# Performance work log

Measured on AMD Instinct MI355X. Metric: run time of the kernel, lower is better.

The kernel has to match this reference:

```python
import jax, jax.numpy as jnp
import numpy as np

B, T, N, D = 16, 24, 2048, 64
L, K = 2, 3  # num_layers, cheb_k


def setup_inputs() -> dict:
    key = jax.random.key(0)
    ks = jax.random.split(key, 6)
    x = jax.random.normal(ks[0], (B, T, N, D), dtype=jnp.float32)
    init_state = jnp.zeros((L, B, N, D), dtype=jnp.float32)
    adj = jax.random.uniform(ks[1], (N, N), dtype=jnp.float32)
    adj = adj / jnp.sum(adj, axis=-1, keepdims=True)  # row-normalized adjacency
    cin = 2 * D
    Wg = jax.random.normal(ks[2], (L, K, cin, 2 * D), dtype=jnp.float32) * (1.0 / np.sqrt(K * cin))
    bg = jnp.zeros((L, 2 * D), dtype=jnp.float32)
    Wu = jax.random.normal(ks[3], (L, K, cin, D), dtype=jnp.float32) * (1.0 / np.sqrt(K * cin))
    bu = jnp.zeros((L, D), dtype=jnp.float32)
    return {"x": x, "init_state": init_state, "adj_matrix": adj,
            "Wg": Wg, "bg": bg, "Wu": Wu, "bu": bu}


def _cheb_supports(adj, k):
    # T0=I, T1=A, Tk = 2*A@T_{k-1} - T_{k-2}
    n = adj.shape[0]
    sup = [jnp.eye(n, dtype=adj.dtype), adj]
    for _ in range(2, k):
        sup.append(2.0 * adj @ sup[-1] - sup[-2])
    return jnp.stack(sup[:k], axis=0)  # [K, N, N]


def _gconv(xs, supports, W, b):
    # xs: [B,N,Cin], supports: [K,N,N], W: [K,Cin,Cout]
    xg = jnp.einsum('knm,bmc->bknc', supports, xs)
    return jnp.einsum('bknc,kco->bno', xg, W) + b


def _cell(x_t, state, supports, Wg_l, bg_l, Wu_l, bu_l):
    ins = jnp.concatenate([x_t, state], axis=-1)  # [B,N,2D]
    zr = jax.nn.sigmoid(_gconv(ins, supports, Wg_l, bg_l))
    z, r = jnp.split(zr, 2, axis=-1)
    cand_in = jnp.concatenate([x_t, z * state], axis=-1)
    hc = jnp.tanh(_gconv(cand_in, supports, Wu_l, bu_l))
    return r * state + (1.0 - r) * hc


def reference(x, init_state, adj_matrix, Wg, bg, Wu, bu):
    supports = _cheb_supports(adj_matrix, K)
    current = x  # [B,T,N,D]
    hiddens = []
    for l in range(L):
        def step(state, x_t, l=l):
            new = _cell(x_t, state, supports, Wg[l], bg[l], Wu[l], bu[l])
            return new, new
        last, seq = jax.lax.scan(step, init_state[l], jnp.swapaxes(current, 0, 1))
        hiddens.append(last)
        current = x + jnp.swapaxes(seq, 0, 1)  # residual over the stacked states
    return current, jnp.stack(hiddens, axis=0)
```

## Files before the change

### kernel.cpp

```cpp
#include <hip/hip_runtime.h>
#include <hip/hip_bf16.h>
#include <math.h>

typedef __bf16 bf16x8 __attribute__((ext_vector_type(8)));
typedef float f32x4 __attribute__((ext_vector_type(4)));
typedef __hip_bfloat16 bf16s;

constexpr int kB = 16, kT = 24, kN = 2048, kD = 64;
constexpr size_t kBND = (size_t)kB * kN * kD;

struct Slot { const void* p0; const void* p1; int astr0, trow0, astr1, trow1, type; };
struct Slots6 { Slot s[6]; };
struct DiffGrp { const bf16s* src; bf16s* oA; bf16s* oA2; };
struct Diff2P { const bf16s* S0; const bf16s* S1; DiffGrp g[2]; int ytPerGrp; };

__device__ __forceinline__ void async_copy16(void* lds, const void* g) {
  __builtin_amdgcn_global_load_lds((const __attribute__((address_space(1))) void*)g,
                                   (__attribute__((address_space(3))) void*)lds,
                                   16, 0, 0);
}


__device__ __forceinline__ void diff2_tile(
    const bf16s* __restrict__ S0, const bf16s* __restrict__ S1,
    const bf16s* __restrict__ src, bf16s* oA, bf16s* oA2,
    int m0, int c0, bf16s* lds)
{
  bf16s* lA  = lds;
  bf16s* lA2 = lds + 4096;
  bf16s* lB  = lds + 8192;
  const int tid = threadIdx.x, lane = tid & 63, wave = tid >> 6;
  const int wm = (wave >> 1) * 32, wn = (wave & 1) * 64;
  const int ra = tid >> 3;
  const int cs = ((tid & 7) ^ (ra & 7)) * 8;
  const int rk0 = ((lane >> 4) ^ (lane & 7)) * 8;
  const int rk1 = ((4 + (lane >> 4)) ^ (lane & 7)) * 8;

  f32x4 acc[2][2][4];
  const f32x4 zero = {0.f, 0.f, 0.f, 0.f};
#pragma unroll
  for (int s = 0; s < 2; ++s)
#pragma unroll
    for (int i = 0; i < 2; ++i)
#pragma unroll
      for (int j = 0; j < 4; ++j) acc[s][i][j] = zero;

  for (int k0 = 0; k0 < 2048; k0 += 64) {
#pragma unroll
    for (int i = 0; i < 2; ++i) {
      async_copy16(lA  + (size_t)(i * 256 + tid) * 8,
                   S0 + (size_t)(m0 + i * 32 + ra) * 2048 + k0 + cs);
      async_copy16(lA2 + (size_t)(i * 256 + tid) * 8,
                   S1 + (size_t)(m0 + i * 32 + ra) * 2048 + k0 + cs);
    }
#pragma unroll
    for (int i = 0; i < 4; ++i)
      async_copy16(lB + (size_t)(i * 256 + tid) * 8,
                   src + (size_t)(c0 + i * 32 + ra) * 2048 + k0 + cs);
    __syncthreads();
#pragma unroll
    for (int ks = 0; ks < 2; ++ks) {
      const int rk = ks ? rk1 : rk0;
      bf16x8 av0[2], av1[2], bv[4];
#pragma unroll
      for (int f = 0; f < 2; ++f) {
        av0[f] = *(const bf16x8*)(lA  + (size_t)(wm + f * 16 + (lane & 15)) * 64 + rk);
        av1[f] = *(const bf16x8*)(lA2 + (size_t)(wm + f * 16 + (lane & 15)) * 64 + rk);
      }
#pragma unroll
      for (int f = 0; f < 4; ++f)
        bv[f] = *(const bf16x8*)(lB + (size_t)(wn + f * 16 + (lane & 15)) * 64 + rk);
#pragma unroll
      for (int i = 0; i < 2; ++i)
#pragma unroll
        for (int j = 0; j < 4; ++j) {
          acc[0][i][j] = __builtin_amdgcn_mfma_f32_16x16x32_bf16(av0[i], bv[j], acc[0][i][j], 0, 0, 0);
          acc[1][i][j] = __builtin_amdgcn_mfma_f32_16x16x32_bf16(av1[i], bv[j], acc[1][i][j], 0, 0, 0);
        }
    }
    __syncthreads();
  }

  const int rq = (lane >> 4) * 4, cl = lane & 15;
#pragma unroll
  for (int sp = 0; sp < 2; ++sp) {
    bf16s* out = sp ? oA2 : oA;
#pragma unroll
    for (int fm = 0; fm < 2; ++fm)
#pragma unroll
      for (int fn = 0; fn < 4; ++fn)
#pragma unroll
        for (int q = 0; q < 4; ++q) {
          int gm = m0 + wm + fm * 16 + rq + q;
          int gc = c0 + wn + fn * 16 + cl;
          out[((size_t)(gc >> 6) * 2048 + gm) * 64 + (gc & 63)] =
              __float2bfloat16(acc[sp][fm][fn][q]);
        }
  }
}

__global__ __launch_bounds__(256) void k_diff2(Diff2P p)
{
  __shared__ bf16s lds[16384];
  const int mb = blockIdx.x;
  const int grp = blockIdx.y / p.ytPerGrp;
  const int cb = blockIdx.y - grp * p.ytPerGrp;
  const DiffGrp G = p.g[grp];
  diff2_tile(p.S0, p.S1, G.src, G.oA, G.oA2, mb * 64, cb * 128, lds);
}

__device__ __forceinline__ void diff_core(
    const bf16s* __restrict__ S, const bf16s* __restrict__ Bsrc,
    int m0, int c0, bf16s* lA, bf16s* lB, f32x4 (&acc)[4][4])
{
  const int tid = threadIdx.x, lane = tid & 63, wave = tid >> 6;
  const int wm = (wave >> 1) * 64, wn = (wave & 1) * 64;
  const f32x4 zero = {0.f, 0.f, 0.f, 0.f};
#pragma unroll
  for (int i = 0; i < 4; ++i)
#pragma unroll
    for (int j = 0; j < 4; ++j) acc[i][j] = zero;

  const int ra = tid >> 3;
  const int cs = ((tid & 7) ^ (ra & 7)) * 8;
  const int rk0 = ((lane >> 4) ^ (lane & 7)) * 8;
  const int rk1 = ((4 + (lane >> 4)) ^ (lane & 7)) * 8;

  for (int k0 = 0; k0 < 2048; k0 += 64) {
#pragma unroll
    for (int i = 0; i < 4; ++i) {
      async_copy16(lA + (size_t)(i * 256 + tid) * 8,
                   S + (size_t)(m0 + i * 32 + ra) * 2048 + k0 + cs);
      async_copy16(lB + (size_t)(i * 256 + tid) * 8,
                   Bsrc + (size_t)(c0 + i * 32 + ra) * 2048 + k0 + cs);
    }
    __syncthreads();
#pragma unroll
    for (int ks = 0; ks < 2; ++ks) {
      const int rk = ks ? rk1 : rk0;
      bf16x8 av[4], bv[4];
#pragma unroll
      for (int f = 0; f < 4; ++f) {
        av[f] = *(const bf16x8*)(lA + (size_t)(wm + f * 16 + (lane & 15)) * 64 + rk);
        bv[f] = *(const bf16x8*)(lB + (size_t)(wn + f * 16 + (lane & 15)) * 64 + rk);
      }
#pragma unroll
      for (int i = 0; i < 4; ++i)
#pragma unroll
        for (int j = 0; j < 4; ++j)
          acc[i][j] = __builtin_amdgcn_mfma_f32_16x16x32_bf16(av[i], bv[j], acc[i][j], 0, 0, 0);
    }
    __syncthreads();
  }
}

__global__ __launch_bounds__(256) void k_a2(
    const bf16s* __restrict__ A, const bf16s* __restrict__ AT, bf16s* A2)
{
  __shared__ bf16s lA[128 * 64];
  __shared__ bf16s lB[128 * 64];
  const int m0 = blockIdx.x * 128, n0 = blockIdx.y * 128;
  f32x4 acc[4][4];
  diff_core(A, AT, m0, n0, lA, lB, acc);
  const int lane = threadIdx.x & 63, wave = threadIdx.x >> 6;
  const int wm = (wave >> 1) * 64, wn = (wave & 1) * 64;
  const int rq = (lane >> 4) * 4, cl = lane & 15;
#pragma unroll
  for (int fm = 0; fm < 4; ++fm)
#pragma unroll
    for (int fn = 0; fn < 4; ++fn)
#pragma unroll
      for (int q = 0; q < 4; ++q) {
        int gm = m0 + wm + fm * 16 + rq + q;
        int gc = n0 + wn + fn * 16 + cl;
        A2[(size_t)gm * 2048 + gc] = __float2bfloat16(2.f * acc[fm][fn][q] - (gm == gc ? 1.f : 0.f));
      }
}

template<int BN>
__device__ __forceinline__ void small_core(
    const Slots6& sl, int m0, const bf16s* __restrict__ W,
    bf16s* lA, bf16s* lB, f32x4 (&acc)[4][BN / 32])
{
  const int tid = threadIdx.x, lane = tid & 63, wave = tid >> 6;
  const int wm = (wave >> 1) * 64, wn = (wave & 1) * (BN / 2);
  const f32x4 zero = {0.f, 0.f, 0.f, 0.f};
#pragma unroll
  for (int i = 0; i < 4; ++i)
#pragma unroll
    for (int j = 0; j < BN / 32; ++j) acc[i][j] = zero;

  const int ra = tid >> 3;
  const int cs = ((tid & 7) ^ (ra & 7)) * 8;
  const int rk0 = ((lane >> 4) ^ (lane & 7)) * 8;
  const int rk1 = ((4 + (lane >> 4)) ^ (lane & 7)) * 8;

#pragma unroll
  for (int ks = 0; ks < 6; ++ks) {
    const Slot sd = sl.s[ks];
    if (sd.type == 0) {
      const bf16s* base = (const bf16s*)sd.p0;
#pragma unroll
      for (int i = 0; i < 4; ++i) {
        int row = m0 + i * 32 + ra;
        size_t roff = ((size_t)(row >> 11) * sd.astr0 + sd.trow0 + (row & 2047)) * 64 + cs;
        async_copy16(lA + (size_t)(i * 256 + tid) * 8, base + roff);
      }
    } else if (sd.type == 1) {
#pragma unroll
      for (int i = 0; i < 4; ++i) {
        int row = m0 + i * 32 + ra;
        size_t roff = ((size_t)(row >> 11) * sd.astr0 + sd.trow0 + (row & 2047)) * 64 + cs;
        const float4* q0 = (const float4*)((const float*)sd.p0 + roff);
        float4 a = q0[0], b = q0[1];
        union { bf16x8 v; bf16s h[8]; } u;
        u.h[0] = __float2bfloat16(a.x); u.h[1] = __float2bfloat16(a.y);
        u.h[2] = __float2bfloat16(a.z); u.h[3] = __float2bfloat16(a.w);
        u.h[4] = __float2bfloat16(b.x); u.h[5] = __float2bfloat16(b.y);
        u.h[6] = __float2bfloat16(b.z); u.h[7] = __float2bfloat16(b.w);
        *(bf16x8*)(lA + (size_t)(i * 256 + tid) * 8) = u.v;
      }
    } else {
#pragma unroll
      for (int i = 0; i < 4; ++i) {
        int row = m0 + i * 32 + ra;
        size_t r0o = ((size_t)(row >> 11) * sd.astr0 + sd.trow0 + (row & 2047)) * 64 + cs;
        size_t r1o = ((size_t)(row >> 11) * sd.astr1 + sd.trow1 + (row & 2047)) * 64 + cs;
        union { bf16x8 v; bf16s h[8]; } a, b, o;
        a.v = *(const bf16x8*)((const bf16s*)sd.p0 + r0o);
        b.v = *(const bf16x8*)((const bf16s*)sd.p1 + r1o);
#pragma unroll
        for (int j = 0; j < 8; ++j)
          o.h[j] = __float2bfloat16(__bfloat162float(a.h[j]) + __bfloat162float(b.h[j]));
        *(bf16x8*)(lA + (size_t)(i * 256 + tid) * 8) = o.v;
      }
    }
#pragma unroll
    for (int i = 0; i < BN / 32; ++i)
      async_copy16(lB + (size_t)(i * 256 + tid) * 8,
                   W + (size_t)(i * 32 + ra) * 384 + ks * 64 + cs);
    __syncthreads();
#pragma unroll
    for (int kss = 0; kss < 2; ++kss) {
      const int rk = kss ? rk1 : rk0;
      bf16x8 av[4], bv[BN / 32];
#pragma unroll
      for (int f = 0; f < 4; ++f)
        av[f] = *(const bf16x8*)(lA + (size_t)(wm + f * 16 + (lane & 15)) * 64 + rk);
#pragma unroll
      for (int f = 0; f < BN / 32; ++f)
        bv[f] = *(const bf16x8*)(lB + (size_t)(wn + f * 16 + (lane & 15)) * 64 + rk);
#pragma unroll
      for (int i = 0; i < 4; ++i)
#pragma unroll
        for (int j = 0; j < BN / 32; ++j)
          acc[i][j] = __builtin_amdgcn_mfma_f32_16x16x32_bf16(av[i], bv[j], acc[i][j], 0, 0, 0);
    }
    __syncthreads();
  }
}

struct LayerG {
  Slots6 sl; const bf16s* W; const float* bias;
  const float* h; bf16s* zh; bf16s* zhT; float* r;
};
__global__ __launch_bounds__(256) void k_gate(LayerG A, LayerG B, int nA)
{
  __shared__ bf16s lA[128 * 64];
  __shared__ bf16s lB[128 * 64];
  const int bx = blockIdx.x;
  const bool isA = bx < nA;
  const LayerG L = isA ? A : B;
  const int m0 = (isA ? bx : bx - nA) * 128;
  f32x4 acc[4][4];
  small_core<128>(L.sl, m0, L.W, lA, lB, acc);
  const int lane = threadIdx.x & 63, wave = threadIdx.x >> 6;
  const int wm = (wave >> 1) * 64, wn = (wave & 1) * 64;
  const int rq = (lane >> 4) * 4, cl = lane & 15;
#pragma unroll
  for (int fm = 0; fm < 4; ++fm)
#pragma unroll
    for (int fn = 0; fn < 4; ++fn) {
      const int o = wn + fn * 16 + cl;
      const float bias = L.bias[o];
#pragma unroll
      for (int q = 0; q < 4; ++q) {
        size_t gm = (size_t)m0 + wm + fm * 16 + rq + q;
        float s = 1.f / (1.f + expf(-(acc[fm][fn][q] + bias)));
        if (o < 64) {
          float zh = s * L.h[gm * 64 + o];
          L.zh[gm * 64 + o] = __float2bfloat16(zh);
          L.zhT[((size_t)((gm >> 11) * 64 + o)) * 2048 + (gm & 2047)] = __float2bfloat16(zh);
        } else {
          L.r[gm * 64 + (o - 64)] = s;
        }
      }
    }
}

__device__ __forceinline__ Slot Sb_d(const void* p0, int astr, int trow) {
  return Slot{p0, nullptr, astr, trow, 0, 0, 0};
}
__device__ __forceinline__ Slot Sf_d(const void* p0, int astr, int trow) {
  return Slot{p0, nullptr, astr, trow, 0, 0, 1};
}
__device__ __forceinline__ Slot S2_d(const void* p0, const void* p1, int astr1, int trow1) {
  return Slot{p0, p1, 2048, 0, astr1, trow1, 2};
}

struct CandP {
  const bf16s *A, *A2;
  const bf16s *zhT0, *zhT1;
  bf16s *sZ0, *sA2Z0, *sZ1, *sA2Z1;
  const float *x;
  const bf16s *zhbf0, *zhbf1, *x1prev;
  const bf16s *AxF, *A2xF, *sAh0, *sA2h0;
  const bf16s *WuT; const float *bu;
  const float *r32_0, *r32_1;
  float *h32_0, *h32_1;
  bf16s *hT0, *hT1, *hbf0, *hbf1;
  bf16s *x1cur;
  float *outCur, *outHid;
  int tA, tB, aA, aB;
};

__global__ __launch_bounds__(256, 2) void k_dcand(CandP P)
{
  __shared__ bf16s lds[16384];
  const int layer = blockIdx.x >> 8;
  if (layer ? !P.aB : !P.aA) return;
  const int lin = blockIdx.x & 255;
  const int mb = (lin & 7) | (((lin >> 6) & 3) << 3);
  const int cb = (lin >> 3) & 7;
  const int m0 = mb * 64, c0 = cb * 128, b0 = cb * 2;
  const int t = layer ? P.tB : P.tA;

  const int tid = threadIdx.x, lane = tid & 63, wave = tid >> 6;
  const int ra = tid >> 3;
  const int cs = ((tid & 7) ^ (ra & 7)) * 8;
  const int rk0 = ((lane >> 4) ^ (lane & 7)) * 8;
  const int rk1 = ((4 + (lane >> 4)) ^ (lane & 7)) * 8;

  diff2_tile(P.A, P.A2, layer ? P.zhT1 : P.zhT0,
             layer ? P.sZ1 : P.sZ0, layer ? P.sA2Z1 : P.sA2Z0,
             m0, c0, lds);
  __syncthreads();

  Slots6 sl;
  if (!layer) {
    sl.s[0] = Sf_d(P.x, kT * 2048, P.tA * 2048);
    sl.s[1] = Sb_d(P.zhbf0, 2048, 0);
    sl.s[2] = Sb_d(P.AxF, kT * 2048, P.tA * 2048);
    sl.s[3] = Sb_d(P.sZ0, 2048, 0);
    sl.s[4] = Sb_d(P.A2xF, kT * 2048, P.tA * 2048);
    sl.s[5] = Sb_d(P.sA2Z0, 2048, 0);
  } else {
    sl.s[0] = Sb_d(P.x1prev, 2048, 0);
    sl.s[1] = Sb_d(P.zhbf1, 2048, 0);
    sl.s[2] = S2_d(P.sAh0, P.AxF, kT * 2048, P.tB * 2048);
    sl.s[3] = Sb_d(P.sZ1, 2048, 0);
    sl.s[4] = S2_d(P.sA2h0, P.A2xF, kT * 2048, P.tB * 2048);
    sl.s[5] = Sb_d(P.sA2Z1, 2048, 0);
  }
  const bf16s* W = P.WuT + (size_t)layer * 64 * 384;
  const float* bias = P.bu + layer * 64;

  bf16s* gA = lds;
  bf16s* gB = lds + 8192;
  const int wmG = (wave >> 1) * 64, wnG = (wave & 1) * 32;
  f32x4 gacc[4][2];
  const f32x4 zero = {0.f, 0.f, 0.f, 0.f};
#pragma unroll
  for (int i = 0; i < 4; ++i)
#pragma unroll
    for (int j = 0; j < 2; ++j) gacc[i][j] = zero;

#pragma unroll
  for (int ks = 0; ks < 6; ++ks) {
    const Slot sd = sl.s[ks];
    if (sd.type == 0) {
      const bf16s* base = (const bf16s*)sd.p0;
#pragma unroll
      for (int i = 0; i < 4; ++i) {
        int vrow = i * 32 + ra;
        size_t gm = (size_t)(b0 + (vrow >> 6)) * 2048 + m0 + (vrow & 63);
        size_t roff = ((gm >> 11) * sd.astr0 + sd.trow0 + (gm & 2047)) * 64 + cs;
        async_copy16(gA + (size_t)(i * 256 + tid) * 8, base + roff);
      }
    } else if (sd.type == 1) {
#pragma unroll
      for (int i = 0; i < 4; ++i) {
        int vrow = i * 32 + ra;
        size_t gm = (size_t)(b0 + (vrow >> 6)) * 2048 + m0 + (vrow & 63);
        size_t roff = ((gm >> 11) * sd.astr0 + sd.trow0 + (gm & 2047)) * 64 + cs;
        const float4* q0 = (const float4*)((const float*)sd.p0 + roff);
        float4 a = q0[0], b = q0[1];
        union { bf16x8 v; bf16s h[8]; } u;
        u.h[0] = __float2bfloat16(a.x); u.h[1] = __float2bfloat16(a.y);
        u.h[2] = __float2bfloat16(a.z); u.h[3] = __float2bfloat16(a.w);
        u.h[4] = __float2bfloat16(b.x); u.h[5] = __float2bfloat16(b.y);
        u.h[6] = __float2bfloat16(b.z); u.h[7] = __float2bfloat16(b.w);
        *(bf16x8*)(gA + (size_t)(i * 256 + tid) * 8) = u.v;
      }
    } else {
#pragma unroll
      for (int i = 0; i < 4; ++i) {
        int vrow = i * 32 + ra;
        size_t gm = (size_t)(b0 + (vrow >> 6)) * 2048 + m0 + (vrow & 63);
        size_t r0o = ((gm >> 11) * sd.astr0 + sd.trow0 + (gm & 2047)) * 64 + cs;
        size_t r1o = ((gm >> 11) * sd.astr1 + sd.trow1 + (gm & 2047)) * 64 + cs;
        union { bf16x8 v; bf16s h[8]; } a, b, o;
        a.v = *(const bf16x8*)((const bf16s*)sd.p0 + r0o);
        b.v = *(const bf16x8*)((const bf16s*)sd.p1 + r1o);
#pragma unroll
        for (int j = 0; j < 8; ++j)
          o.h[j] = __float2bfloat16(__bfloat162float(a.h[j]) + __bfloat162float(b.h[j]));
        *(bf16x8*)(gA + (size_t)(i * 256 + tid) * 8) = o.v;
      }
    }
#pragma unroll
    for (int i = 0; i < 2; ++i)
      async_copy16(gB + (size_t)(i * 256 + tid) * 8,
                   W + (size_t)(i * 32 + ra) * 384 + ks * 64 + cs);
    __syncthreads();
#pragma unroll
    for (int kss = 0; kss < 2; ++kss) {
      const int rk = kss ? rk1 : rk0;
      bf16x8 av[4], bv[2];
#pragma unroll
      for (int f = 0; f < 4; ++f)
        av[f] = *(const bf16x8*)(gA + (size_t)(wmG + f * 16 + (lane & 15)) * 64 + rk);
#pragma unroll
      for (int f = 0; f < 2; ++f)
        bv[f] = *(const bf16x8*)(gB + (size_t)(wnG + f * 16 + (lane & 15)) * 64 + rk);
#pragma unroll
      for (int i = 0; i < 4; ++i)
#pragma unroll
        for (int j = 0; j < 2; ++j)
          gacc[i][j] = __builtin_amdgcn_mfma_f32_16x16x32_bf16(av[i], bv[j], gacc[i][j], 0, 0, 0);
    }
    __syncthreads();
  }

  const float* r32 = layer ? P.r32_1 : P.r32_0;
  float* h32 = layer ? P.h32_1 : P.h32_0;
  bf16s* hT  = layer ? P.hT1  : P.hT0;
  bf16s* hbf = layer ? P.hbf1 : P.hbf0;
  const int rq = (lane >> 4) * 4, cl = lane & 15;
#pragma unroll
  for (int fm = 0; fm < 4; ++fm)
#pragma unroll
    for (int fn = 0; fn < 2; ++fn) {
      const int d = wnG + fn * 16 + cl;
      const float bias_d = bias[d];
#pragma unroll
      for (int q = 0; q < 4; ++q) {
        int vrow = wmG + fm * 16 + rq + q;
        size_t gm = (size_t)(b0 + (vrow >> 6)) * 2048 + m0 + (vrow & 63);
        float hc = tanhf(gacc[fm][fn][q] + bias_d);
        float r = r32[gm * 64 + d];
        float h = h32[gm * 64 + d];
        float hn = r * h + (1.f - r) * hc;
        h32[gm * 64 + d] = hn;
        int b = (int)(gm >> 11), n = (int)(gm & 2047);
        hT[((size_t)(b * 64 + d)) * 2048 + n] = __float2bfloat16(hn);
        hbf[gm * 64 + d] = __float2bfloat16(hn);
        size_t xi = (((size_t)b * kT + t) * 2048 + n) * 64 + d;
        if (!layer) {
          P.x1cur[gm * 64 + d] = __float2bfloat16(P.x[xi] + hn);
          if (t == kT - 1) P.outHid[gm * 64 + d] = hn;
        } else {
          P.outCur[xi] = P.x[xi] + hn;
          if (t == kT - 1) (P.outHid + kBND)[gm * 64 + d] = hn;
        }
      }
    }
}

__global__ __launch_bounds__(256) void transpose_cvt(
    const float* in, bf16s* out, int nrows, int ncols,
    size_t in_ostride, size_t out_ostride)
{
  __shared__ float tile[64][65];
  const int r0 = blockIdx.x * 64, c0 = blockIdx.y * 64;
  in  += (size_t)blockIdx.z * in_ostride;
  out += (size_t)blockIdx.z * out_ostride;
  const int tx = threadIdx.x & 63, ty = threadIdx.x >> 6;
#pragma unroll
  for (int i = 0; i < 64; i += 4)
    tile[ty + i][tx] = in[(size_t)(r0 + ty + i) * ncols + c0 + tx];
  __syncthreads();
#pragma unroll
  for (int i = 0; i < 64; i += 4)
    out[(size_t)(c0 + ty + i) * nrows + r0 + tx] = __float2bfloat16(tile[tx][ty + i]);
}

__global__ __launch_bounds__(256) void k_cvt(const float* in, bf16s* out, int n)
{
  int i = blockIdx.x * 256 + threadIdx.x;
  if (i < n) out[i] = __float2bfloat16(in[i]);
}

__global__ __launch_bounds__(256) void k_repack(
    const float* Wg, const float* Wu, bf16s* WgT, bf16s* WuT)
{
  int idx = blockIdx.x * 256 + threadIdx.x;
  if (idx < 2 * 3 * 128 * 128) {
    int o = idx & 127, cin = (idx >> 7) & 127, k = (idx >> 14) % 3, l = idx / 49152;
    WgT[((size_t)(l * 128 + o)) * 384 + (2 * k + (cin >> 6)) * 64 + (cin & 63)] =
        __float2bfloat16(Wg[idx]);
  }
  if (idx < 2 * 3 * 128 * 64) {
    int o = idx & 63, cin = (idx >> 6) & 127, k = (idx >> 13) % 3, l = idx / 24576;
    WuT[((size_t)(l * 64 + o)) * 384 + (2 * k + (cin >> 6)) * 64 + (cin & 63)] =
        __float2bfloat16(Wu[idx]);
  }
}

__global__ __launch_bounds__(256) void init_layer(
    const float* ist_l, float* h32, bf16s* hT, bf16s* h_bf)
{
  size_t idx = (size_t)blockIdx.x * 256 + threadIdx.x;
  if (idx >= kBND) return;
  int d = (int)(idx & 63);
  size_t row = idx >> 6;
  int n = (int)(row & 2047), b = (int)(row >> 11);
  float h = ist_l[idx];
  h32[idx] = h;
  hT[((size_t)(b * 64 + d)) * 2048 + n] = __float2bfloat16(h);
  h_bf[idx] = __float2bfloat16(h);
}

extern "C" void kernel_launch(void* const* d_in, const int* in_sizes, int n_in,
                              void* d_out, int out_size, void* d_ws, size_t ws_size,
                              hipStream_t stream)
{
  (void)in_sizes; (void)n_in; (void)out_size; (void)ws_size;
  const float* x   = (const float*)d_in[0];
  const float* ist = (const float*)d_in[1];
  const float* adj = (const float*)d_in[2];
  const float* Wg  = (const float*)d_in[3];
  const float* bg  = (const float*)d_in[4];
  const float* Wu  = (const float*)d_in[5];
  const float* bu  = (const float*)d_in[6];
  float* outCur = (float*)d_out;
  float* outHid = outCur + (size_t)kB * kT * kN * kD;

  char* p = (char*)d_ws;
  auto carve = [&](size_t bytes) { char* q = p; p += (bytes + 255) & ~(size_t)255; return q; };
  bf16s* A_bf  = (bf16s*)carve((size_t)2048 * 2048 * 2);
  bf16s* A2_bf = (bf16s*)carve((size_t)2048 * 2048 * 2);
  bf16s* WgT   = (bf16s*)carve((size_t)2 * 128 * 384 * 2);
  bf16s* WuT   = (bf16s*)carve((size_t)2 * 64 * 384 * 2);
  float* h32b  = (float*)carve(2 * kBND * 4);
  float* r32b  = (float*)carve(2 * kBND * 4);
  bf16s* hTb   = (bf16s*)carve(2 * kBND * 2);
  bf16s* hbfb  = (bf16s*)carve(2 * kBND * 2);
  bf16s* zhTb  = (bf16s*)carve(2 * kBND * 2);
  bf16s* zhbfb = (bf16s*)carve(2 * kBND * 2);
  bf16s* x1b   = (bf16s*)carve(2 * kBND * 2);
  bf16s* sAh0  = (bf16s*)carve(kBND * 2);
  bf16s* sA2h0 = (bf16s*)carve(kBND * 2);
  bf16s* sAh1  = (bf16s*)carve(kBND * 2);
  bf16s* sA2h1 = (bf16s*)carve(kBND * 2);
  bf16s* sZ0   = (bf16s*)carve(kBND * 2);
  bf16s* sA2Z0 = (bf16s*)carve(kBND * 2);
  bf16s* sZ1   = (bf16s*)carve(kBND * 2);
  bf16s* sA2Z1 = (bf16s*)carve(kBND * 2);
  const size_t xTfull = (size_t)kB * kT * kD * kN * 2;
  bf16s* AxF  = (bf16s*)carve(xTfull);
  bf16s* A2xF = (bf16s*)carve(xTfull);
  bf16s* xTh  = (bf16s*)carve(xTfull / 2);
  bf16s* AT_bf = AxF;

  float* h32_0 = h32b;   float* h32_1 = h32b + kBND;
  float* r32_0 = r32b;   float* r32_1 = r32b + kBND;
  bf16s* hT0 = hTb;      bf16s* hT1 = hTb + kBND;
  bf16s* hbf0 = hbfb;    bf16s* hbf1 = hbfb + kBND;
  bf16s* zhT0 = zhTb;    bf16s* zhT1 = zhTb + kBND;
  bf16s* zhbf0 = zhbfb;  bf16s* zhbf1 = zhbfb + kBND;

  k_cvt<<<dim3((2048 * 2048 + 255) / 256), 256, 0, stream>>>(adj, A_bf, 2048 * 2048);
  transpose_cvt<<<dim3(32, 32, 1), 256, 0, stream>>>(adj, AT_bf, 2048, 2048, 0, 0);
  k_a2<<<dim3(16, 16, 1), 256, 0, stream>>>(A_bf, AT_bf, A2_bf);
  k_repack<<<dim3(384), 256, 0, stream>>>(Wg, Wu, WgT, WuT);
  init_layer<<<dim3((int)(kBND / 256)), 256, 0, stream>>>(ist, h32_0, hT0, hbf0);
  init_layer<<<dim3((int)(kBND / 256)), 256, 0, stream>>>(ist + kBND, h32_1, hT1, hbf1);

  for (int h = 0; h < 2; ++h) {
    size_t off = (size_t)h * 8 * kT * 131072;
    transpose_cvt<<<dim3(32, 1, 8 * kT), 256, 0, stream>>>(x + off, xTh, 2048, 64, 131072, 131072);
    Diff2P dp; dp.S0 = A_bf; dp.S1 = A2_bf; dp.ytPerGrp = 96;
    dp.g[0] = DiffGrp{xTh, AxF + off, A2xF + off};
    dp.g[1] = dp.g[0];
    k_diff2<<<dim3(32, 96), 256, 0, stream>>>(dp);
  }

  auto Sb = [](const void* p0, int astr, int trow) { return Slot{p0, nullptr, astr, trow, 0, 0, 0}; };
  auto Sf = [](const void* p0, int astr, int trow) { return Slot{p0, nullptr, astr, trow, 0, 0, 1}; };
  auto S2 = [](const void* p0, const void* p1, int astr1, int trow1) {
    return Slot{p0, p1, 2048, 0, astr1, trow1, 2};
  };

  for (int s = 0; s <= kT; ++s) {
    const bool aA = (s < kT), aB = (s >= 1);
    const int tA = s, tB = s - 1;
    const int nA = aA ? 256 : 0, nB = aB ? 256 : 0;
    bf16s* x1cur  = x1b + (size_t)(s & 1) * kBND;
    bf16s* x1prev = x1b + (size_t)((s - 1) & 1) * kBND;

    {
      Diff2P dp; dp.S0 = A_bf; dp.S1 = A2_bf; dp.ytPerGrp = 8;
      int ng = 1;
      dp.g[0] = DiffGrp{hT0, sAh0, sA2h0};
      dp.g[1] = aB ? DiffGrp{hT1, sAh1, sA2h1} : dp.g[0];
      if (aB) ng = 2;
      k_diff2<<<dim3(32, 8 * ng), 256, 0, stream>>>(dp);
    }

    {
      LayerG GA = {}, GB = {};
      if (aA) {
        GA.sl.s[0] = Sf(x, kT * 2048, tA * 2048);
        GA.sl.s[1] = Sb(hbf0, 2048, 0);
        GA.sl.s[2] = Sb(AxF, kT * 2048, tA * 2048);
        GA.sl.s[3] = Sb(sAh0, 2048, 0);
        GA.sl.s[4] = Sb(A2xF, kT * 2048, tA * 2048);
        GA.sl.s[5] = Sb(sA2h0, 2048, 0);
        GA.W = WgT; GA.bias = bg; GA.h = h32_0; GA.zh = zhbf0; GA.zhT = zhT0; GA.r = r32_0;
      }
      if (aB) {
        GB.sl.s[0] = Sb(x1prev, 2048, 0);
        GB.sl.s[1] = Sb(hbf1, 2048, 0);
        GB.sl.s[2] = S2(sAh0, AxF, kT * 2048, tB * 2048);
        GB.sl.s[3] = Sb(sAh1, 2048, 0);
        GB.sl.s[4] = S2(sA2h0, A2xF, kT * 2048, tB * 2048);
        GB.sl.s[5] = Sb(sA2h1, 2048, 0);
        GB.W = WgT + (size_t)128 * 384; GB.bias = bg + 128;
        GB.h = h32_1; GB.zh = zhbf1; GB.zhT = zhT1; GB.r = r32_1;
      }
      k_gate<<<dim3(nA + nB), 256, 0, stream>>>(GA, GB, nA);
    }

    {
      CandP P;
      P.A = A_bf; P.A2 = A2_bf;
      P.zhT0 = zhT0; P.zhT1 = zhT1;
      P.sZ0 = sZ0; P.sA2Z0 = sA2Z0; P.sZ1 = sZ1; P.sA2Z1 = sA2Z1;
      P.x = x; P.zhbf0 = zhbf0; P.zhbf1 = zhbf1; P.x1prev = x1prev;
      P.AxF = AxF; P.A2xF = A2xF; P.sAh0 = sAh0; P.sA2h0 = sA2h0;
      P.WuT = WuT; P.bu = bu;
      P.r32_0 = r32_0; P.r32_1 = r32_1;
      P.h32_0 = h32_0; P.h32_1 = h32_1;
      P.hT0 = hT0; P.hT1 = hT1; P.hbf0 = hbf0; P.hbf1 = hbf1;
      P.x1cur = x1cur; P.outCur = outCur; P.outHid = outHid;
      P.tA = tA; P.tB = tB; P.aA = aA ? 1 : 0; P.aB = aB ? 1 : 0;
      k_dcand<<<dim3(512), 256, 0, stream>>>(P);
    }
  }
}
```

Before: 4.883 ms.

## Replace fused dual-support diffusion kernel with 128x128 single-support tiles and block swizzle

The diffusion GEMM kernel that computed both A·X and A2·X per 64-row tile, sharing the B operand in LDS, is replaced by k_diff. k_diff assigns each block a 128x128 tile of either A or A2 and uses a 1D grid with a block-index swizzle meant to improve L2 locality. This gives up reuse of the source tile across both supports in exchange for larger square tiles and more independent blocks. The two init_layer launches are also merged into one, and the slot staging code is moved into a helper function.

```diff
diff --git a/kernel.cpp b/kernel.cpp
--- a/kernel.cpp
+++ b/kernel.cpp
@@ -12,7 +12,7 @@
 struct Slot { const void* p0; const void* p1; int astr0, trow0, astr1, trow1, type; };
 struct Slots6 { Slot s[6]; };
 struct DiffGrp { const bf16s* src; bf16s* oA; bf16s* oA2; };
-struct Diff2P { const bf16s* S0; const bf16s* S1; DiffGrp g[2]; int ytPerGrp; };
+struct DiffP { const bf16s* S0; const bf16s* S1; DiffGrp g[2]; int nCb; };
 
 __device__ __forceinline__ void async_copy16(void* lds, const void* g) {
   __builtin_amdgcn_global_load_lds((const __attribute__((address_space(1))) void*)g,
@@ -20,6 +20,113 @@
                                    16, 0, 0);
 }
 
+
+__device__ __forceinline__ void diff_core(
+    const bf16s* __restrict__ S, const bf16s* __restrict__ Bsrc,
+    int m0, int c0, bf16s* lA, bf16s* lB, f32x4 (&acc)[4][4])
+{
+  const int tid = threadIdx.x, lane = tid & 63, wave = tid >> 6;
+  const int wm = (wave >> 1) * 64, wn = (wave & 1) * 64;
+  const f32x4 zero = {0.f, 0.f, 0.f, 0.f};
+#pragma unroll
+  for (int i = 0; i < 4; ++i)
+#pragma unroll
+    for (int j = 0; j < 4; ++j) acc[i][j] = zero;
+
+  const int ra = tid >> 3;
+  const int cs = ((tid & 7) ^ (ra & 7)) * 8;
+  const int rk0 = ((lane >> 4) ^ (lane & 7)) * 8;
+  const int rk1 = ((4 + (lane >> 4)) ^ (lane & 7)) * 8;
+
+  for (int k0 = 0; k0 < 2048; k0 += 64) {
+#pragma unroll
+    for (int i = 0; i < 4; ++i) {
+      async_copy16(lA + (size_t)(i * 256 + tid) * 8,
+                   S + (size_t)(m0 + i * 32 + ra) * 2048 + k0 + cs);
+      async_copy16(lB + (size_t)(i * 256 + tid) * 8,
+                   Bsrc + (size_t)(c0 + i * 32 + ra) * 2048 + k0 + cs);
+    }
+    __syncthreads();
+#pragma unroll
+    for (int ks = 0; ks < 2; ++ks) {
+      const int rk = ks ? rk1 : rk0;
+      bf16x8 av[4], bv[4];
+#pragma unroll
+      for (int f = 0; f < 4; ++f) {
+        av[f] = *(const bf16x8*)(lA + (size_t)(wm + f * 16 + (lane & 15)) * 64 + rk);
+        bv[f] = *(const bf16x8*)(lB + (size_t)(wn + f * 16 + (lane & 15)) * 64 + rk);
+      }
+#pragma unroll
+      for (int i = 0; i < 4; ++i)
+#pragma unroll
+        for (int j = 0; j < 4; ++j)
+          acc[i][j] = __builtin_amdgcn_mfma_f32_16x16x32_bf16(av[i], bv[j], acc[i][j], 0, 0, 0);
+    }
+    __syncthreads();
+  }
+}
+
+__device__ __forceinline__ void diff_tile(
+    const bf16s* __restrict__ S, const bf16s* __restrict__ src, bf16s* out,
+    int m0, int c0, bf16s* lA, bf16s* lB)
+{
+  f32x4 acc[4][4];
+  diff_core(S, src, m0, c0, lA, lB, acc);
+  const int lane = threadIdx.x & 63, wave = threadIdx.x >> 6;
+  const int wm = (wave >> 1) * 64, wn = (wave & 1) * 64;
+  const int rq = (lane >> 4) * 4, cl = lane & 15;
+#pragma unroll
+  for (int fm = 0; fm < 4; ++fm)
+#pragma unroll
+    for (int fn = 0; fn < 4; ++fn)
+#pragma unroll
+      for (int q = 0; q < 4; ++q) {
+        int gm = m0 + wm + fm * 16 + rq + q;
+        int gc = c0 + wn + fn * 16 + cl;
+        size_t off = ((size_t)(gc >> 6) * 2048 + gm) * 64 + (gc & 63);
+        out[off] = __float2bfloat16(acc[fm][fn][q]);
+      }
+}
+
+__global__ __launch_bounds__(256) void k_diff(DiffP p)
+{
+  __shared__ bf16s lA[128 * 64];
+  __shared__ bf16s lB[128 * 64];
+  const int nb = gridDim.x;
+  const int swz = (blockIdx.x & 7) * (nb >> 3) + (blockIdx.x >> 3);
+  const int mi = swz & 31;
+  const int gc = swz >> 5;
+  const int grp = gc / p.nCb;
+  const int cb = gc - grp * p.nCb;
+  const bf16s* S = (mi >> 4) ? p.S1 : p.S0;
+  const int m0 = (mi & 15) * 128;
+  const DiffGrp G = p.g[grp];
+  bf16s* out = (mi >> 4) ? G.oA2 : G.oA;
+  diff_tile(S, G.src, out, m0, cb * 128, lA, lB);
+}
+
+__global__ __launch_bounds__(256) void k_a2(
+    const bf16s* __restrict__ A, const bf16s* __restrict__ AT, bf16s* A2)
+{
+  __shared__ bf16s lA[128 * 64];
+  __shared__ bf16s lB[128 * 64];
+  const int m0 = blockIdx.x * 128, n0 = blockIdx.y * 128;
+  f32x4 acc[4][4];
+  diff_core(A, AT, m0, n0, lA, lB, acc);
+  const int lane = threadIdx.x & 63, wave = threadIdx.x >> 6;
+  const int wm = (wave >> 1) * 64, wn = (wave & 1) * 64;
+  const int rq = (lane >> 4) * 4, cl = lane & 15;
+#pragma unroll
+  for (int fm = 0; fm < 4; ++fm)
+#pragma unroll
+    for (int fn = 0; fn < 4; ++fn)
+#pragma unroll
+      for (int q = 0; q < 4; ++q) {
+        int gm = m0 + wm + fm * 16 + rq + q;
+        int gc = n0 + wn + fn * 16 + cl;
+        A2[(size_t)gm * 2048 + gc] = __float2bfloat16(2.f * acc[fm][fn][q] - (gm == gc ? 1.f : 0.f));
+      }
+}
 
 __device__ __forceinline__ void diff2_tile(
     const bf16s* __restrict__ S0, const bf16s* __restrict__ S1,
@@ -99,82 +206,14 @@
   }
 }
 
-__global__ __launch_bounds__(256) void k_diff2(Diff2P p)
-{
-  __shared__ bf16s lds[16384];
-  const int mb = blockIdx.x;
-  const int grp = blockIdx.y / p.ytPerGrp;
-  const int cb = blockIdx.y - grp * p.ytPerGrp;
-  const DiffGrp G = p.g[grp];
-  diff2_tile(p.S0, p.S1, G.src, G.oA, G.oA2, mb * 64, cb * 128, lds);
-}
-
-__device__ __forceinline__ void diff_core(
-    const bf16s* __restrict__ S, const bf16s* __restrict__ Bsrc,
-    int m0, int c0, bf16s* lA, bf16s* lB, f32x4 (&acc)[4][4])
-{
-  const int tid = threadIdx.x, lane = tid & 63, wave = tid >> 6;
-  const int wm = (wave >> 1) * 64, wn = (wave & 1) * 64;
-  const f32x4 zero = {0.f, 0.f, 0.f, 0.f};
-#pragma unroll
-  for (int i = 0; i < 4; ++i)
-#pragma unroll
-    for (int j = 0; j < 4; ++j) acc[i][j] = zero;
-
-  const int ra = tid >> 3;
-  const int cs = ((tid & 7) ^ (ra & 7)) * 8;
-  const int rk0 = ((lane >> 4) ^ (lane & 7)) * 8;
-  const int rk1 = ((4 + (lane >> 4)) ^ (lane & 7)) * 8;
-
-  for (int k0 = 0; k0 < 2048; k0 += 64) {
-#pragma unroll
-    for (int i = 0; i < 4; ++i) {
-      async_copy16(lA + (size_t)(i * 256 + tid) * 8,
-                   S + (size_t)(m0 + i * 32 + ra) * 2048 + k0 + cs);
-      async_copy16(lB + (size_t)(i * 256 + tid) * 8,
-                   Bsrc + (size_t)(c0 + i * 32 + ra) * 2048 + k0 + cs);
-    }
-    __syncthreads();
-#pragma unroll
-    for (int ks = 0; ks < 2; ++ks) {
-      const int rk = ks ? rk1 : rk0;
-      bf16x8 av[4], bv[4];
-#pragma unroll
-      for (int f = 0; f < 4; ++f) {
-        av[f] = *(const bf16x8*)(lA + (size_t)(wm + f * 16 + (lane & 15)) * 64 + rk);
-        bv[f] = *(const bf16x8*)(lB + (size_t)(wn + f * 16 + (lane & 15)) * 64 + rk);
-      }
-#pragma unroll
-      for (int i = 0; i < 4; ++i)
-#pragma unroll
-        for (int j = 0; j < 4; ++j)
-          acc[i][j] = __builtin_amdgcn_mfma_f32_16x16x32_bf16(av[i], bv[j], acc[i][j], 0, 0, 0);
-    }
-    __syncthreads();
-  }
-}
-
-__global__ __launch_bounds__(256) void k_a2(
-    const bf16s* __restrict__ A, const bf16s* __restrict__ AT, bf16s* A2)
-{
-  __shared__ bf16s lA[128 * 64];
-  __shared__ bf16s lB[128 * 64];
-  const int m0 = blockIdx.x * 128, n0 = blockIdx.y * 128;
-  f32x4 acc[4][4];
-  diff_core(A, AT, m0, n0, lA, lB, acc);
-  const int lane = threadIdx.x & 63, wave = threadIdx.x >> 6;
-  const int wm = (wave >> 1) * 64, wn = (wave & 1) * 64;
-  const int rq = (lane >> 4) * 4, cl = lane & 15;
-#pragma unroll
-  for (int fm = 0; fm < 4; ++fm)
-#pragma unroll
-    for (int fn = 0; fn < 4; ++fn)
-#pragma unroll
-      for (int q = 0; q < 4; ++q) {
-        int gm = m0 + wm + fm * 16 + rq + q;
-        int gc = n0 + wn + fn * 16 + cl;
-        A2[(size_t)gm * 2048 + gc] = __float2bfloat16(2.f * acc[fm][fn][q] - (gm == gc ? 1.f : 0.f));
-      }
+__device__ __forceinline__ Slot Sb_d(const void* p0, int astr, int trow) {
+  return Slot{p0, nullptr, astr, trow, 0, 0, 0};
+}
+__device__ __forceinline__ Slot Sf_d(const void* p0, int astr, int trow) {
+  return Slot{p0, nullptr, astr, trow, 0, 0, 1};
+}
+__device__ __forceinline__ Slot S2_d(const void* p0, const void* p1, int astr1, int trow1) {
+  return Slot{p0, p1, 2048, 0, astr1, trow1, 2};
 }
 
 template<int BN>
@@ -298,14 +337,49 @@
     }
 }
 
-__device__ __forceinline__ Slot Sb_d(const void* p0, int astr, int trow) {
-  return Slot{p0, nullptr, astr, trow, 0, 0, 0};
-}
-__device__ __forceinline__ Slot Sf_d(const void* p0, int astr, int trow) {
-  return Slot{p0, nullptr, astr, trow, 0, 0, 1};
-}
-__device__ __forceinline__ Slot S2_d(const void* p0, const void* p1, int astr1, int trow1) {
-  return Slot{p0, p1, 2048, 0, astr1, trow1, 2};
+__device__ __forceinline__ void stage_slotA(
+    const Slot& sd, bf16s* gA, int b0, int m0, int tid, int ra, int cs)
+{
+  if (sd.type == 0) {
+    const bf16s* base = (const bf16s*)sd.p0;
+#pragma unroll
+    for (int i = 0; i < 4; ++i) {
+      int vrow = i * 32 + ra;
+      size_t gm = (size_t)(b0 + (vrow >> 6)) * 2048 + m0 + (vrow & 63);
+      size_t roff = ((gm >> 11) * sd.astr0 + sd.trow0 + (gm & 2047)) * 64 + cs;
+      async_copy16(gA + (size_t)(i * 256 + tid) * 8, base + roff);
+    }
+  } else if (sd.type == 1) {
+#pragma unroll
+    for (int i = 0; i < 4; ++i) {
+      int vrow = i * 32 + ra;
+      size_t gm = (size_t)(b0 + (vrow >> 6)) * 2048 + m0 + (vrow & 63);
+      size_t roff = ((gm >> 11) * sd.astr0 + sd.trow0 + (gm & 2047)) * 64 + cs;
+      const float4* q0 = (const float4*)((const float*)sd.p0 + roff);
+      float4 a = q0[0], b = q0[1];
+      union { bf16x8 v; bf16s h[8]; } u;
+      u.h[0] = __float2bfloat16(a.x); u.h[1] = __float2bfloat16(a.y);
+      u.h[2] = __float2bfloat16(a.z); u.h[3] = __float2bfloat16(a.w);
+      u.h[4] = __float2bfloat16(b.x); u.h[5] = __float2bfloat16(b.y);
+      u.h[6] = __float2bfloat16(b.z); u.h[7] = __float2bfloat16(b.w);
+      *(bf16x8*)(gA + (size_t)(i * 256 + tid) * 8) = u.v;
+    }
+  } else {
+#pragma unroll
+    for (int i = 0; i < 4; ++i) {
+      int vrow = i * 32 + ra;
+      size_t gm = (size_t)(b0 + (vrow >> 6)) * 2048 + m0 + (vrow & 63);
+      size_t r0o = ((gm >> 11) * sd.astr0 + sd.trow0 + (gm & 2047)) * 64 + cs;
+      size_t r1o = ((gm >> 11) * sd.astr1 + sd.trow1 + (gm & 2047)) * 64 + cs;
+      union { bf16x8 v; bf16s h[8]; } a, b, o;
+      a.v = *(const bf16x8*)((const bf16s*)sd.p0 + r0o);
+      b.v = *(const bf16x8*)((const bf16s*)sd.p1 + r1o);
+#pragma unroll
+      for (int j = 0; j < 8; ++j)
+        o.h[j] = __float2bfloat16(__bfloat162float(a.h[j]) + __bfloat162float(b.h[j]));
+      *(bf16x8*)(gA + (size_t)(i * 256 + tid) * 8) = o.v;
+    }
+  }
 }
 
 struct CandP {
@@ -377,47 +451,7 @@
 
 #pragma unroll
   for (int ks = 0; ks < 6; ++ks) {
-    const Slot sd = sl.s[ks];
-    if (sd.type == 0) {
-      const bf16s* base = (const bf16s*)sd.p0;
-#pragma unroll
-      for (int i = 0; i < 4; ++i) {
-        int vrow = i * 32 + ra;
-        size_t gm = (size_t)(b0 + (vrow >> 6)) * 2048 + m0 + (vrow & 63);
-        size_t roff = ((gm >> 11) * sd.astr0 + sd.trow0 + (gm & 2047)) * 64 + cs;
-        async_copy16(gA + (size_t)(i * 256 + tid) * 8, base + roff);
-      }
-    } else if (sd.type == 1) {
-#pragma unroll
-      for (int i = 0; i < 4; ++i) {
-        int vrow = i * 32 + ra;
-        size_t gm = (size_t)(b0 + (vrow >> 6)) * 2048 + m0 + (vrow & 63);
-        size_t roff = ((gm >> 11) * sd.astr0 + sd.trow0 + (gm & 2047)) * 64 + cs;
-        const float4* q0 = (const float4*)((const float*)sd.p0 + roff);
-        float4 a = q0[0], b = q0[1];
-        union { bf16x8 v; bf16s h[8]; } u;
-        u.h[0] = __float2bfloat16(a.x); u.h[1] = __float2bfloat16(a.y);
-        u.h[2] = __float2bfloat16(a.z); u.h[3] = __float2bfloat16(a.w);
-        u.h[4] = __float2bfloat16(b.x); u.h[5] = __float2bfloat16(b.y);
-        u.h[6] = __float2bfloat16(b.z); u.h[7] = __float2bfloat16(b.w);
-        *(bf16x8*)(gA + (size_t)(i * 256 + tid) * 8) = u.v;
-      }
-    } else {
-#pragma unroll
-      for (int i = 0; i < 4; ++i) {
-        int vrow = i * 32 + ra;
-        size_t gm = (size_t)(b0 + (vrow >> 6)) * 2048 + m0 + (vrow & 63);
-        size_t r0o = ((gm >> 11) * sd.astr0 + sd.trow0 + (gm & 2047)) * 64 + cs;
-        size_t r1o = ((gm >> 11) * sd.astr1 + sd.trow1 + (gm & 2047)) * 64 + cs;
-        union { bf16x8 v; bf16s h[8]; } a, b, o;
-        a.v = *(const bf16x8*)((const bf16s*)sd.p0 + r0o);
-        b.v = *(const bf16x8*)((const bf16s*)sd.p1 + r1o);
-#pragma unroll
-        for (int j = 0; j < 8; ++j)
-          o.h[j] = __float2bfloat16(__bfloat162float(a.h[j]) + __bfloat162float(b.h[j]));
-        *(bf16x8*)(gA + (size_t)(i * 256 + tid) * 8) = o.v;
-      }
-    }
+    stage_slotA(sl.s[ks], gA, b0, m0, tid, ra, cs);
 #pragma unroll
     for (int i = 0; i < 2; ++i)
       async_copy16(gB + (size_t)(i * 256 + tid) * 8,
@@ -517,9 +551,14 @@
   }
 }
 
-__global__ __launch_bounds__(256) void init_layer(
-    const float* ist_l, float* h32, bf16s* hT, bf16s* h_bf)
-{
+__global__ __launch_bounds__(256) void init_layer2(
+    const float* ist, float* h32b, bf16s* hTb, bf16s* hbfb)
+{
+  const int l = blockIdx.y;
+  const float* ist_l = ist + (size_t)l * kBND;
+  float* h32 = h32b + (size_t)l * kBND;
+  bf16s* hT  = hTb  + (size_t)l * kBND;
+  bf16s* hbf = hbfb + (size_t)l * kBND;
   size_t idx = (size_t)blockIdx.x * 256 + threadIdx.x;
   if (idx >= kBND) return;
   int d = (int)(idx & 63);
@@ -528,7 +567,7 @@
   float h = ist_l[idx];
   h32[idx] = h;
   hT[((size_t)(b * 64 + d)) * 2048 + n] = __float2bfloat16(h);
-  h_bf[idx] = __float2bfloat16(h);
+  hbf[idx] = __float2bfloat16(h);
 }
 
 extern "C" void kernel_launch(void* const* d_in, const int* in_sizes, int n_in,
@@ -584,16 +623,15 @@
   transpose_cvt<<<dim3(32, 32, 1), 256, 0, stream>>>(adj, AT_bf, 2048, 2048, 0, 0);
   k_a2<<<dim3(16, 16, 1), 256, 0, stream>>>(A_bf, AT_bf, A2_bf);
   k_repack<<<dim3(384), 256, 0, stream>>>(Wg, Wu, WgT, WuT);
-  init_layer<<<dim3((int)(kBND / 256)), 256, 0, stream>>>(ist, h32_0, hT0, hbf0);
-  init_layer<<<dim3((int)(kBND / 256)), 256, 0, stream>>>(ist + kBND, h32_1, hT1, hbf1);
+  init_layer2<<<dim3((int)(kBND / 256), 2), 256, 0, stream>>>(ist, h32b, hTb, hbfb);
 
   for (int h = 0; h < 2; ++h) {
     size_t off = (size_t)h * 8 * kT * 131072;
     transpose_cvt<<<dim3(32, 1, 8 * kT), 256, 0, stream>>>(x + off, xTh, 2048, 64, 131072, 131072);
-    Diff2P dp; dp.S0 = A_bf; dp.S1 = A2_bf; dp.ytPerGrp = 96;
+    DiffP dp; dp.S0 = A_bf; dp.S1 = A2_bf; dp.nCb = 96;
     dp.g[0] = DiffGrp{xTh, AxF + off, A2xF + off};
     dp.g[1] = dp.g[0];
-    k_diff2<<<dim3(32, 96), 256, 0, stream>>>(dp);
+    k_diff<<<dim3(32 * 96), 256, 0, stream>>>(dp);
   }
 
   auto Sb = [](const void* p0, int astr, int trow) { return Slot{p0, nullptr, astr, trow, 0, 0, 0}; };
@@ -610,12 +648,12 @@
     bf16s* x1prev = x1b + (size_t)((s - 1) & 1) * kBND;
 
     {
-      Diff2P dp; dp.S0 = A_bf; dp.S1 = A2_bf; dp.ytPerGrp = 8;
+      DiffP dp; dp.S0 = A_bf; dp.S1 = A2_bf; dp.nCb = 8;
       int ng = 1;
       dp.g[0] = DiffGrp{hT0, sAh0, sA2h0};
       dp.g[1] = aB ? DiffGrp{hT1, sAh1, sA2h1} : dp.g[0];
       if (aB) ng = 2;
-      k_diff2<<<dim3(32, 8 * ng), 256, 0, stream>>>(dp);
+      k_diff<<<dim3(32 * 8 * ng), 256, 0, stream>>>(dp);
     }
 
     {
```

Result: faster. 4.778 ms (-2.2%).
